# Performance work log

Measured on AMD Instinct MI355X. Metric: run time of the kernel, lower is better.

The kernel has to match this reference:

```python
import jax, jax.numpy as jnp
import numpy as np

N = 100000      # nodes (PF candidates)
E = 1600000     # edges, avg degree 16
CONT = 6        # continuous features
H = 32          # hidden_dim
PDGS = [1, 2, 11, 13, 22, 130, 211]


def _p(k, shape):
    return jax.random.normal(k, shape, jnp.float32) * 0.1


def setup_inputs() -> dict:
    key = jax.random.key(0)
    ks = jax.random.split(key, 24)
    x_cont = jax.random.normal(ks[0], (N, CONT), jnp.float32)
    pdg = jnp.array(PDGS, jnp.int32)[jax.random.randint(ks[1], (N,), 0, 7)]
    sign = jax.random.randint(ks[2], (N,), 0, 2) * 2 - 1
    charge = jax.random.randint(ks[3], (N,), -1, 2)
    pv = jax.random.randint(ks[4], (N,), 0, 8)
    x_cat = jnp.stack([pdg * sign, charge, pv], axis=1).astype(jnp.int32)
    edge_index = jax.random.randint(ks[5], (2, E), 0, N, jnp.int32)
    batch = jnp.zeros((N,), jnp.int32)
    return {
        "x_cont": x_cont, "x_cat": x_cat, "edge_index": edge_index, "batch": batch,
        "W_cont": _p(ks[6], (CONT, H // 2)), "b_cont": jnp.zeros((H // 2,), jnp.float32),
        "T_chrg": _p(ks[7], (3, H // 4)), "T_pdg": _p(ks[8], (7, H // 4)), "T_pv": _p(ks[9], (8, H // 4)),
        "W_cat": _p(ks[10], (3 * H // 4, H // 2)), "b_cat": jnp.zeros((H // 2,), jnp.float32),
        "W_enc": _p(ks[11], (H, H)), "b_enc": jnp.zeros((H,), jnp.float32),
        "g_all": jnp.ones((H,), jnp.float32), "be_all": jnp.zeros((H,), jnp.float32),
        "W_msg": _p(ks[12], (2 * H, H)), "b_msg": jnp.zeros((H,), jnp.float32),
        "g_conv": jnp.ones((H,), jnp.float32), "be_conv": jnp.zeros((H,), jnp.float32),
        "W_out1": _p(ks[13], (H, H // 2)), "b_out1": jnp.zeros((H // 2,), jnp.float32),
        "W_out2": _p(ks[14], (H // 2, 1)), "b_out2": jnp.zeros((1,), jnp.float32),
    }


def _batchnorm(x, gamma, beta, eps=1e-5):
    # training-mode BatchNorm1d: biased batch stats over the node axis
    mu = jnp.mean(x, axis=0)
    var = jnp.mean(jnp.square(x - mu), axis=0)
    return (x - mu) * jax.lax.rsqrt(var + eps) * gamma + beta


def reference(x_cont, x_cat, edge_index, batch,
              W_cont, b_cont, T_chrg, T_pdg, T_pv, W_cat, b_cat,
              W_enc, b_enc, g_all, be_all, W_msg, b_msg, g_conv, be_conv,
              W_out1, b_out1, W_out2, b_out2):
    elu = jax.nn.elu
    emb_cont = elu(x_cont @ W_cont + b_cont)                      # [N, H/2]
    emb_chrg = T_chrg[x_cat[:, 1] + 1]                            # [N, H/4]
    emb_pv = T_pv[x_cat[:, 2]]                                    # [N, H/4]
    pdg_remap = jnp.abs(x_cat[:, 0])
    for i, pdgval in enumerate(PDGS):  # fixed small constant loop, as in original
        pdg_remap = jnp.where(pdg_remap == pdgval, jnp.int32(i), pdg_remap)
    emb_pdg = T_pdg[pdg_remap]                                    # [N, H/4]
    emb_cat = elu(jnp.concatenate([emb_chrg, emb_pdg, emb_pv], axis=1) @ W_cat + b_cat)
    emb = elu(jnp.concatenate([emb_cat, emb_cont], axis=1) @ W_enc + b_enc)
    emb = _batchnorm(emb, g_all, be_all)                          # [N, H]
    # EdgeConv: m_ij = nn([x_i, x_j - x_i]), aggregate by max over incoming edges
    src, dst = edge_index[0], edge_index[1]
    x_i = emb[dst]
    x_j = emb[src]
    msg = jnp.concatenate([x_i, x_j - x_i], axis=1) @ W_msg + b_msg   # [E, H]
    agg = jax.ops.segment_max(msg, dst, num_segments=N)
    agg = jnp.where(jnp.isfinite(agg), agg, 0.0)                  # nodes w/o in-edges -> 0
    emb = emb + _batchnorm(agg, g_conv, be_conv)
    out = elu(emb @ W_out1 + b_out1) @ W_out2 + b_out2            # [N, 1]
    return out.squeeze(-1)
```

## Files before the change

### kernel.cpp

```cpp
#include <hip/hip_runtime.h>
#include <hip/hip_bf16.h>

#define NN 100000
#define EE 1600000
#define NB_SCAN 391

#define NBUCK 782
#define CPAD  16
#define NCB   128
#define NPART 391
#define NE4   400000
#define BCAP  2560

typedef __hip_bfloat16 bf16_t;
typedef int int4v __attribute__((ext_vector_type(4)));
typedef float f4 __attribute__((ext_vector_type(4)));

#define PARB  600000
#define EMB   604480
#define PBUF  3804480
#define QBUF  7004480
#define ABUF  10204480
#define SOFF  13404480
#define CURS  (SOFF + 256)
#define BASEO (CURS + 12512)
#define ROWP  (BASEO + 1024)
#define SRCL  (ROWP + 100002)

#define O_WCONT 0
#define O_BCONT 96
#define O_TCHRG 112
#define O_TPDG  136
#define O_TPV   192
#define O_WCAT  256
#define O_BCAT  640
#define O_WENC  656
#define O_BENC  1680
#define O_GALL  1712
#define O_BEALL 1744
#define O_WMSG  1776
#define O_BMSG  3824
#define O_GCONV 3856
#define O_BECONV 3888
#define O_WOUT1 3920
#define O_BOUT1 4432
#define O_WOUT2 4448
#define O_BOUT2 4464
#define NPAR    4465

__device__ __forceinline__ float bf(unsigned short u) {
    return __uint_as_float(((unsigned)u) << 16);
}
__device__ __forceinline__ f4 elu4(f4 v) {
    f4 r;
    r.x = v.x > 0.0f ? v.x : expm1f(v.x);
    r.y = v.y > 0.0f ? v.y : expm1f(v.y);
    r.z = v.z > 0.0f ? v.z : expm1f(v.z);
    r.w = v.w > 0.0f ? v.w : expm1f(v.w);
    return r;
}
__device__ __forceinline__ f4 f4max(f4 a, f4 b) {
    f4 r;
    r.x = fmaxf(a.x, b.x); r.y = fmaxf(a.y, b.y);
    r.z = fmaxf(a.z, b.z); r.w = fmaxf(a.w, b.w);
    return r;
}

struct InitArgs {
    const void* p[19];
    const unsigned short* wdet;
    int*        flagw;
    float*      par;
    int*        curs;
    float*      stats;
};

__global__ __launch_bounds__(256) void k_init(InitArgs a)
{
    const int offs[20] = {O_WCONT,O_BCONT,O_TCHRG,O_TPDG,O_TPV,O_WCAT,O_BCAT,O_WENC,
                          O_BENC,O_GALL,O_BEALL,O_WMSG,O_BMSG,O_GCONV,O_BECONV,
                          O_WOUT1,O_BOUT1,O_WOUT2,O_BOUT2,NPAR};
    __shared__ int sflag;
    int b = blockIdx.x, tid = threadIdx.x;
    int g = b * 256 + tid;
    if (g < NBUCK * CPAD) a.curs[g] = 0;
    if (g < 128) a.stats[g] = 0.0f;
    if (b == 0) {
        if (tid == 0) sflag = 0;
        __syncthreads();
        int bad = 0;
        for (int i = tid; i < 1024; i += 256) {
            unsigned e = (a.wdet[i] >> 7) & 0xFFu;
            if (e >= 137u) bad = 1;
        }
        if (bad) atomicOr(&sflag, 1);
        __syncthreads();
        int f32 = sflag;
        if (tid == 0) *a.flagw = f32;
        for (int i = tid; i < NPAR; i += 256) {
            int t = 0;
            while (offs[t + 1] <= i) t++;
            int l = i - offs[t];
            const void* s = a.p[t];
            a.par[i] = f32 ? ((const float*)s)[l] : bf(((const unsigned short*)s)[l]);
        }
    }
}

__global__ __launch_bounds__(256, 1) void k_fusedA(
    const int* __restrict__ eidx, int* __restrict__ curs,
    const void* __restrict__ xc, const int* __restrict__ x_cat,
    const float* __restrict__ par, const int* __restrict__ flag,
    float* __restrict__ emb)
{
    __shared__ f4 sWc4[24];
    __shared__ f4 sbc4[4];
    __shared__ f4 sTc4[6], sTp4[14], sTv4[16];
    __shared__ f4 sWcat4[96];
    __shared__ f4 sbcat4[4];
    __shared__ f4 sWe4[256];
    __shared__ f4 sbe4[8];
    int tid = threadIdx.x;
    int b = blockIdx.x;

    if (b < NCB) {
        __shared__ int cnt[NBUCK];
        for (int i = tid; i < NBUCK; i += 256) cnt[i] = 0;
        __syncthreads();
        const int4v* dst4 = (const int4v*)(eidx + EE);
        int i0 = b * (NE4 / NCB);
        int i1 = i0 + (NE4 / NCB);
        for (int i = i0 + tid; i < i1; i += 256) {
            int4v d = __builtin_nontemporal_load(&dst4[i]);
            atomicAdd(&cnt[d.x >> 7], 1);
            atomicAdd(&cnt[d.y >> 7], 1);
            atomicAdd(&cnt[d.z >> 7], 1);
            atomicAdd(&cnt[d.w >> 7], 1);
        }
        __syncthreads();
        for (int i = tid; i < NBUCK; i += 256) {
            int c = cnt[i];
            if (c) atomicAdd(&curs[i * CPAD], c);
        }
        return;
    }

    {
        float* s;
        s=(float*)sWc4;   for(int i=tid;i<96;  i+=256) s[i]=par[O_WCONT+i];
        s=(float*)sbc4;   for(int i=tid;i<16;  i+=256) s[i]=par[O_BCONT+i];
        s=(float*)sTc4;   for(int i=tid;i<24;  i+=256) s[i]=par[O_TCHRG+i];
        s=(float*)sTp4;   for(int i=tid;i<56;  i+=256) s[i]=par[O_TPDG+i];
        s=(float*)sTv4;   for(int i=tid;i<64;  i+=256) s[i]=par[O_TPV+i];
        s=(float*)sWcat4; for(int i=tid;i<384; i+=256) s[i]=par[O_WCAT+i];
        s=(float*)sbcat4; for(int i=tid;i<16;  i+=256) s[i]=par[O_BCAT+i];
        s=(float*)sWe4;   for(int i=tid;i<1024;i+=256) s[i]=par[O_WENC+i];
        s=(float*)sbe4;   for(int i=tid;i<32;  i+=256) s[i]=par[O_BENC+i];
    }
    __syncthreads();

    int n = (b - NCB) * 256 + tid;
    if (n >= NN) return;

    float x0,x1,x2,x3,x4,x5;
    if (*flag) {
        const float* xr = (const float*)xc + (size_t)n * 6;
        x0=xr[0]; x1=xr[1]; x2=xr[2]; x3=xr[3]; x4=xr[4]; x5=xr[5];
    } else {
        const unsigned* xr = (const unsigned*)xc + (size_t)n * 3;
        unsigned w0=xr[0], w1=xr[1], w2=xr[2];
        x0=__uint_as_float(w0<<16); x1=__uint_as_float(w0 & 0xFFFF0000u);
        x2=__uint_as_float(w1<<16); x3=__uint_as_float(w1 & 0xFFFF0000u);
        x4=__uint_as_float(w2<<16); x5=__uint_as_float(w2 & 0xFFFF0000u);
    }

    f4 ec[4];
    #pragma unroll
    for (int g = 0; g < 4; g++) {
        f4 a = sbc4[g];
        a += x0 * sWc4[0*4+g]; a += x1 * sWc4[1*4+g]; a += x2 * sWc4[2*4+g];
        a += x3 * sWc4[3*4+g]; a += x4 * sWc4[4*4+g]; a += x5 * sWc4[5*4+g];
        ec[g] = elu4(a);
    }

    int c0 = x_cat[n*3+0], c1 = x_cat[n*3+1], c2 = x_cat[n*3+2];
    int a0 = c0 < 0 ? -c0 : c0;
    int pi = (a0==1)?0:(a0==2)?1:(a0==11)?2:(a0==13)?3:(a0==22)?4:(a0==130)?5:6;
    int ci = c1 + 1;

    f4 t0a = sTc4[ci*2],  t0b = sTc4[ci*2+1];
    f4 t1a = sTp4[pi*2],  t1b = sTp4[pi*2+1];
    f4 t2a = sTv4[c2*2],  t2b = sTv4[c2*2+1];

    f4 ecat[4];
    #pragma unroll
    for (int g = 0; g < 4; g++) {
        f4 a = sbcat4[g];
        #pragma unroll
        for (int k = 0; k < 4; k++) a += t0a[k] * sWcat4[(k     )*4+g];
        #pragma unroll
        for (int k = 0; k < 4; k++) a += t0b[k] * sWcat4[(4 + k )*4+g];
        #pragma unroll
        for (int k = 0; k < 4; k++) a += t1a[k] * sWcat4[(8 + k )*4+g];
        #pragma unroll
        for (int k = 0; k < 4; k++) a += t1b[k] * sWcat4[(12 + k)*4+g];
        #pragma unroll
        for (int k = 0; k < 4; k++) a += t2a[k] * sWcat4[(16 + k)*4+g];
        #pragma unroll
        for (int k = 0; k < 4; k++) a += t2b[k] * sWcat4[(20 + k)*4+g];
        ecat[g] = elu4(a);
    }

    f4* o = (f4*)(emb + (size_t)n * 32);
    #pragma unroll
    for (int cg = 0; cg < 8; cg++) {
        f4 a = sbe4[cg];
        #pragma unroll
        for (int kg = 0; kg < 4; kg++) {
            #pragma unroll
            for (int k = 0; k < 4; k++)
                a += ecat[kg][k] * sWe4[(kg*4+k)*8 + cg];
        }
        #pragma unroll
        for (int kg = 0; kg < 4; kg++) {
            #pragma unroll
            for (int k = 0; k < 4; k++)
                a += ec[kg][k] * sWe4[(16 + kg*4+k)*8 + cg];
        }
        o[cg] = elu4(a);
    }
}

__global__ __launch_bounds__(1024) void k_scan782(int* __restrict__ curs,
                                                  int* __restrict__ base,
                                                  int* __restrict__ rowp)
{
    __shared__ int s[1024];
    int tid = threadIdx.x;
    int v = (tid < NBUCK) ? curs[tid * CPAD] : 0;
    s[tid] = v;
    __syncthreads();
    for (int off = 1; off < 1024; off <<= 1) {
        int x = (tid >= off) ? s[tid - off] : 0;
        __syncthreads();
        s[tid] += x;
        __syncthreads();
    }
    if (tid < NBUCK) {
        int bexc = s[tid] - v;
        base[tid] = bexc;
        curs[tid * CPAD] = bexc;
    }
    if (tid == NBUCK - 1) base[NBUCK] = s[tid];
    if (tid == 0) rowp[NN] = EE;
}

__global__ __launch_bounds__(256, 1) void k_partition(
    const int* __restrict__ eidx, int* __restrict__ curs, int* __restrict__ pe)
{
    __shared__ int cnt[NBUCK];
    __shared__ int start[NBUCK];
    int tid = threadIdx.x;
    int b = blockIdx.x;
    for (int i = tid; i < NBUCK; i += 256) cnt[i] = 0;
    __syncthreads();

    const int4v* src4 = (const int4v*)eidx;
    const int4v* dst4 = (const int4v*)(eidx + EE);
    int i0 = b << 10;
    int i1 = i0 + 1024; if (i1 > NE4) i1 = NE4;

    for (int i = i0 + tid; i < i1; i += 256) {
        int4v d = dst4[i];
        atomicAdd(&cnt[d.x >> 7], 1);
        atomicAdd(&cnt[d.y >> 7], 1);
        atomicAdd(&cnt[d.z >> 7], 1);
        atomicAdd(&cnt[d.w >> 7], 1);
    }
    __syncthreads();
    for (int i = tid; i < NBUCK; i += 256) {
        int c = cnt[i];
        start[i] = c ? atomicAdd(&curs[i * CPAD], c) : 0;
    }
    __syncthreads();
    for (int i = tid; i < NBUCK; i += 256) cnt[i] = 0;
    __syncthreads();
    for (int i = i0 + tid; i < i1; i += 256) {
        int4v s = src4[i];
        int4v d = dst4[i];
        int bk, r;
        bk = d.x >> 7; r = atomicAdd(&cnt[bk], 1); pe[start[bk] + r] = (s.x << 7) | (d.x & 127);
        bk = d.y >> 7; r = atomicAdd(&cnt[bk], 1); pe[start[bk] + r] = (s.y << 7) | (d.y & 127);
        bk = d.z >> 7; r = atomicAdd(&cnt[bk], 1); pe[start[bk] + r] = (s.z << 7) | (d.z & 127);
        bk = d.w >> 7; r = atomicAdd(&cnt[bk], 1); pe[start[bk] + r] = (s.w << 7) | (d.w & 127);
    }
}

__global__ __launch_bounds__(256) void k_fusedB(
    const int* __restrict__ cbase, const int* __restrict__ pe,
    int* __restrict__ rowp, int* __restrict__ srcl,
    const float* __restrict__ emb, float* __restrict__ stats)
{
    __shared__ int stage[BCAP];
    __shared__ int cnt[128], sc[128], ex[128];
    __shared__ float ls[64];
    int tid = threadIdx.x;
    int b = blockIdx.x;
    if (b < NBUCK) {
        int beg = cbase[b], end = cbase[b + 1];
        int m = end - beg;
        if (tid < 128) cnt[tid] = 0;
        __syncthreads();
        for (int i = tid; i < m; i += 256) {
            int p = pe[beg + i];
            if (i < BCAP) stage[i] = p;
            atomicAdd(&cnt[p & 127], 1);
        }
        __syncthreads();
        if (tid < 128) sc[tid] = cnt[tid];
        __syncthreads();
        for (int off = 1; off < 128; off <<= 1) {
            int x = (tid >= off && tid < 128) ? sc[tid - off] : 0;
            __syncthreads();
            if (tid < 128) sc[tid] += x;
            __syncthreads();
        }
        if (tid < 128) {
            int e0 = sc[tid] - cnt[tid];
            ex[tid] = e0;
            int node = b * 128 + tid;
            if (node < NN) rowp[node] = beg + e0;
            cnt[tid] = 0;
        }
        __syncthreads();
        for (int i = tid; i < m; i += 256) {
            int p = (i < BCAP) ? stage[i] : pe[beg + i];
            int dl = p & 127;
            int r = atomicAdd(&cnt[dl], 1);
            srcl[beg + ex[dl] + r] = p >> 7;
        }
        return;
    }
    if (tid < 64) ls[tid] = 0.0f;
    __syncthreads();
    int sb = b - NBUCK;
    int idx = sb * 256 + tid;
    int stride = 512 * 256;
    int c = idx & 31;
    float sum = 0.0f, q = 0.0f;
    for (int i = idx; i < NN * 32; i += stride) {
        float v = emb[i];
        sum += v; q += v * v;
    }
    sum += __shfl_xor(sum, 32);
    q   += __shfl_xor(q, 32);
    if ((tid & 63) < 32) {
        atomicAdd(&ls[c], sum);
        atomicAdd(&ls[32 + c], q);
    }
    __syncthreads();
    if (tid < 64) atomicAdd(&stats[tid], ls[tid]);
}

__global__ __launch_bounds__(256, 1) void k_fusedC(
    const float* __restrict__ par, const float* __restrict__ stats,
    const float* __restrict__ emb, float* __restrict__ P, float* __restrict__ Q)
{
    __shared__ f4 sWP4[256], sWQ4[256];
    __shared__ f4 sbP4[8], sbQ4[8];
    __shared__ float ssc[32], ssh[32];
    int tid = threadIdx.x;
    int b = blockIdx.x;
    if (tid < 32) {
        float mu  = stats[tid] * (1.0f / NN);
        float var = stats[32 + tid] * (1.0f / NN) - mu * mu;
        float s   = par[O_GALL + tid] * rsqrtf(var + 1e-5f);
        ssc[tid] = s;
        ssh[tid] = par[O_BEALL + tid] - mu * s;
    }
    __syncthreads();
    {
        float* wp = (float*)sWP4;
        float* wq = (float*)sWQ4;
        for (int e = tid; e < 1024; e += 256) {
            int k = e >> 5;
            float w1 = par[O_WMSG + e];
            float w2 = par[O_WMSG + 1024 + e];
            wp[e] = ssc[k] * (w1 - w2);
            wq[e] = ssc[k] * w2;
        }
    }
    if (tid < 32) {
        float aP = par[O_BMSG + tid], aQ = 0.0f;
        for (int k = 0; k < 32; k++) {
            float w1 = par[O_WMSG + k*32 + tid];
            float w2 = par[O_WMSG + (k+32)*32 + tid];
            aP += ssh[k] * (w1 - w2);
            aQ += ssh[k] * w2;
        }
        ((float*)sbP4)[tid] = aP;
        ((float*)sbQ4)[tid] = aQ;
    }
    __syncthreads();

    int n = b * 256 + tid;
    if (n >= NN) return;

    const f4* er = (const f4*)(emb + (size_t)n * 32);
    f4 e[8];
    #pragma unroll
    for (int g = 0; g < 8; g++) e[g] = er[g];

    f4* pr = (f4*)(P + (size_t)n * 32);
    f4* qr = (f4*)(Q + (size_t)n * 32);
    #pragma unroll
    for (int cg = 0; cg < 8; cg++) {
        f4 aP = sbP4[cg];
        f4 aQ = sbQ4[cg];
        #pragma unroll
        for (int kg = 0; kg < 8; kg++) {
            #pragma unroll
            for (int k = 0; k < 4; k++) {
                float ek = e[kg][k];
                aP += ek * sWP4[(kg*4+k)*8 + cg];
                aQ += ek * sWQ4[(kg*4+k)*8 + cg];
            }
        }
        pr[cg] = aP;
        qr[cg] = aQ;
    }
}

__global__ __launch_bounds__(256) void k_gather(
    const int* __restrict__ rowp, const int* __restrict__ srcl,
    const float* __restrict__ Q, const float* __restrict__ P,
    float* __restrict__ agg)
{
    int tid = threadIdx.x;
    int lane = tid & 63;
    int wave = tid >> 6;
    int n = blockIdx.x * 4 + wave;
    int slice = lane >> 3;
    int cg    = lane & 7;
    int beg = rowp[n], end = rowp[n + 1];
    const f4* Q4 = (const f4*)Q;

    f4 pv = (f4){0.f, 0.f, 0.f, 0.f};
    if (lane < 8 && end > beg) pv = ((const f4*)P)[(size_t)n * 8 + lane];

    f4 m = {-INFINITY, -INFINITY, -INFINITY, -INFINITY};
    for (int e = beg + slice; e < end; e += 32) {
        int e1 = min(e + 8,  end - 1);
        int e2 = min(e + 16, end - 1);
        int e3 = min(e + 24, end - 1);
        int s0 = __builtin_nontemporal_load(&srcl[e]);
        int s1 = __builtin_nontemporal_load(&srcl[e1]);
        int s2 = __builtin_nontemporal_load(&srcl[e2]);
        int s3 = __builtin_nontemporal_load(&srcl[e3]);
        f4 q0 = Q4[(size_t)s0 * 8 + cg];
        f4 q1 = Q4[(size_t)s1 * 8 + cg];
        f4 q2 = Q4[(size_t)s2 * 8 + cg];
        f4 q3 = Q4[(size_t)s3 * 8 + cg];
        q0 = f4max(q0, q1);
        q2 = f4max(q2, q3);
        m = f4max(m, f4max(q0, q2));
    }
    #pragma unroll
    for (int off = 8; off < 64; off <<= 1) {
        m.x = fmaxf(m.x, __shfl_xor(m.x, off));
        m.y = fmaxf(m.y, __shfl_xor(m.y, off));
        m.z = fmaxf(m.z, __shfl_xor(m.z, off));
        m.w = fmaxf(m.w, __shfl_xor(m.w, off));
    }
    if (lane < 8) {
        f4 o;
        if (end > beg) o = m + pv;
        else           o = (f4){0.f, 0.f, 0.f, 0.f};
        ((f4*)agg)[(size_t)n * 8 + lane] = o;
    }
}

__global__ __launch_bounds__(256) void k_stats(const float* __restrict__ xin,
                                               float* __restrict__ outsums, int count)
{
    __shared__ float ls[64];
    int tid = threadIdx.x;
    if (tid < 64) ls[tid] = 0.0f;
    __syncthreads();
    int idx = blockIdx.x * 256 + tid;
    int stride = gridDim.x * 256;
    int c = idx & 31;
    float s = 0.0f, q = 0.0f;
    for (int i = idx; i < count; i += stride) {
        float v = xin[i];
        s += v; q += v * v;
    }
    s += __shfl_xor(s, 32);
    q += __shfl_xor(q, 32);
    if ((tid & 63) < 32) {
        atomicAdd(&ls[c], s);
        atomicAdd(&ls[32 + c], q);
    }
    __syncthreads();
    if (tid < 64) atomicAdd(&outsums[tid], ls[tid]);
}

__global__ __launch_bounds__(256, 1) void k_out(
    const float* __restrict__ emb, const float* __restrict__ agg,
    const float* __restrict__ par, const float* __restrict__ stats,
    const int* __restrict__ flag, void* __restrict__ out)
{
    __shared__ f4 sW14[128];
    __shared__ f4 sb14[4], sW24[4];
    __shared__ f4 sc14[8], sh14[8], sc24[8], sh24[8];
    __shared__ float sb2s;
    int tid = threadIdx.x;
    {
        float* s = (float*)sW14;
        for (int i = tid; i < 512; i += 256) s[i] = par[O_WOUT1 + i];
    }
    if (tid < 16) {
        ((float*)sb14)[tid] = par[O_BOUT1 + tid];
        ((float*)sW24)[tid] = par[O_WOUT2 + tid];
    }
    if (tid < 32) {
        float mu  = stats[tid] * (1.0f / NN);
        float var = stats[32 + tid] * (1.0f / NN) - mu * mu;
        float s   = par[O_GALL + tid] * rsqrtf(var + 1e-5f);
        ((float*)sc14)[tid] = s;
        ((float*)sh14)[tid] = par[O_BEALL + tid] - mu * s;
        float mu2  = stats[64 + tid] * (1.0f / NN);
        float var2 = stats[96 + tid] * (1.0f / NN) - mu2 * mu2;
        float s2   = par[O_GCONV + tid] * rsqrtf(var2 + 1e-5f);
        ((float*)sc24)[tid] = s2;
        ((float*)sh24)[tid] = par[O_BECONV + tid] - mu2 * s2;
    }
    if (tid == 0) sb2s = par[O_BOUT2];
    __syncthreads();

    int n = blockIdx.x * 256 + tid;
    if (n >= NN) return;

    const f4* er = (const f4*)(emb + (size_t)n * 32);
    const f4* ar = (const f4*)(agg + (size_t)n * 32);
    f4 h[8];
    #pragma unroll
    for (int g = 0; g < 8; g++) {
        f4 ev = er[g];
        f4 av = ar[g];
        h[g] = ev * sc14[g] + sh14[g] + av * sc24[g] + sh24[g];
    }
    f4 o1[4];
    #pragma unroll
    for (int g = 0; g < 4; g++) {
        f4 acc = sb14[g];
        #pragma unroll
        for (int kg = 0; kg < 8; kg++) {
            #pragma unroll
            for (int k = 0; k < 4; k++)
                acc += h[kg][k] * sW14[(kg*4+k)*4 + g];
        }
        o1[g] = elu4(acc);
    }
    float acc = sb2s;
    #pragma unroll
    for (int g = 0; g < 4; g++) {
        f4 p = o1[g] * sW24[g];
        acc += p.x + p.y + p.z + p.w;
    }

    if (*flag) ((float*)out)[n] = acc;
    else       ((bf16_t*)out)[n] = __float2bfloat16(acc);
}

extern "C" void kernel_launch(void* const* d_in, const int* in_sizes, int n_in,
                              void* d_out, int out_size, void* d_ws, size_t ws_size,
                              hipStream_t stream)
{
    const void* x_cont = d_in[0];
    const int* x_cat = (const int*)d_in[1];
    const int* eidx  = (const int*)d_in[2];

    float* ws    = (float*)d_ws;
    float* par   = ws + PARB;
    float* emb   = ws + EMB;
    float* P     = ws + PBUF;
    float* Q     = ws + QBUF;
    float* agg   = ws + ABUF;
    int*   pe    = (int*)(ws + ABUF);
    float* stats = ws + SOFF;
    int*   flag  = (int*)(stats + 128);
    int*   curs  = (int*)(ws + CURS);
    int*   base  = (int*)(ws + BASEO);
    int*   rowp  = (int*)(ws + ROWP);
    int*   srcl  = (int*)(ws + SRCL);

    InitArgs ia;
    for (int t = 0; t < 19; t++) ia.p[t] = d_in[4 + t];
    ia.wdet = (const unsigned short*)d_in[11];
    ia.flagw = flag; ia.par = par; ia.curs = curs; ia.stats = stats;
    k_init<<<NB_SCAN, 256, 0, stream>>>(ia);

    k_fusedA<<<NCB + NB_SCAN, 256, 0, stream>>>(eidx, curs, x_cont, x_cat,
                                                par, flag, emb);
    k_scan782<<<1, 1024, 0, stream>>>(curs, base, rowp);
    k_partition<<<NPART, 256, 0, stream>>>(eidx, curs, pe);
    k_fusedB<<<NBUCK + 512, 256, 0, stream>>>(base, pe, rowp, srcl, emb, stats);
    k_fusedC<<<NB_SCAN, 256, 0, stream>>>(par, stats, emb, P, Q);
    k_gather<<<NN / 4, 256, 0, stream>>>(rowp, srcl, Q, P, agg);
    k_stats<<<512, 256, 0, stream>>>(agg, stats + 64, NN * 32);
    k_out<<<NB_SCAN, 256, 0, stream>>>(emb, agg, par, stats, flag, d_out);
}
```

Baseline: 294.5 us.

## Fuse edge partition with embedding and fold BN stats into producers

Replaces the separate count, scan and partition passes with a single-pass partition into fixed-capacity buckets (4096 slots each), with an atomic overflow list handled later. Embedding BatchNorm stats are computed inside the embedding kernel, and the aggregate stats are accumulated in the gather kernel into 64 partial slots. CSR build is merged with the P/Q precompute, so the pipeline goes from nine launches to five. The risks are an overflow-list scan that every bucket block must walk, extra shared and global atomics, and int2 row pointers.

```diff
diff --git a/kernel.cpp b/kernel.cpp
--- a/kernel.cpp
+++ b/kernel.cpp
@@ -7,9 +7,10 @@
 
 #define NBUCK 782
 #define CPAD  16
-#define NCB   128
 #define NPART 391
 #define NE4   400000
+#define CAP   4096
+#define CAPSH 12
 #define BCAP  2560
 
 typedef __hip_bfloat16 bf16_t;
@@ -22,10 +23,12 @@
 #define QBUF  7004480
 #define ABUF  10204480
 #define SOFF  13404480
-#define CURS  (SOFF + 256)
-#define BASEO (CURS + 12512)
-#define ROWP  (BASEO + 1024)
-#define SRCL  (ROWP + 100002)
+#define PART2 (SOFF + 256)
+#define CURS  (PART2 + 4096)
+#define ROWP2 (CURS + 12512)
+#define OFLB  (ROWP2 + 200000)
+#define PEB   (OFLB + 3200004)
+#define SRCB  (PEB + 3203072)
 
 #define O_WCONT 0
 #define O_BCONT 96
@@ -73,6 +76,9 @@
     float*      par;
     int*        curs;
     float*      stats;
+    float*      part;
+    int*        ofl;
+    int*        tcur;
 };
 
 __global__ __launch_bounds__(256) void k_init(InitArgs a)
@@ -83,8 +89,10 @@
     __shared__ int sflag;
     int b = blockIdx.x, tid = threadIdx.x;
     int g = b * 256 + tid;
-    if (g < NBUCK * CPAD) a.curs[g] = 0;
+    if (g < NBUCK) a.curs[g * CPAD] = g << CAPSH;
+    if (g < 4096) a.part[g] = 0.0f;
     if (g < 128) a.stats[g] = 0.0f;
+    if (g == 0) { a.ofl[0] = 0; *a.tcur = NBUCK << CAPSH; }
     if (b == 0) {
         if (tid == 0) sflag = 0;
         __syncthreads();
@@ -107,310 +115,295 @@
     }
 }
 
-__global__ __launch_bounds__(256, 1) void k_fusedA(
+struct SMemPart { int cnt[NBUCK]; int start[NBUCK]; };
+struct SMemEmb  { float wc[96], bc[16], tc[24], tp[56], tv[64],
+                  wcat[384], bcat[16], we[1024], be[32], ls[64]; };
+union SMemA { SMemPart p; SMemEmb e; };
+
+__global__ __launch_bounds__(256, 1) void k_fA(
     const int* __restrict__ eidx, int* __restrict__ curs,
+    int* __restrict__ pe, int* __restrict__ ofl, int2* __restrict__ ofl2,
     const void* __restrict__ xc, const int* __restrict__ x_cat,
     const float* __restrict__ par, const int* __restrict__ flag,
-    float* __restrict__ emb)
+    float* __restrict__ emb, float* __restrict__ stats)
 {
-    __shared__ f4 sWc4[24];
-    __shared__ f4 sbc4[4];
-    __shared__ f4 sTc4[6], sTp4[14], sTv4[16];
-    __shared__ f4 sWcat4[96];
-    __shared__ f4 sbcat4[4];
-    __shared__ f4 sWe4[256];
-    __shared__ f4 sbe4[8];
+    __shared__ alignas(16) SMemA sm;
     int tid = threadIdx.x;
     int b = blockIdx.x;
 
-    if (b < NCB) {
-        __shared__ int cnt[NBUCK];
-        for (int i = tid; i < NBUCK; i += 256) cnt[i] = 0;
-        __syncthreads();
+    if (b < NPART) {
+        for (int i = tid; i < NBUCK; i += 256) sm.p.cnt[i] = 0;
+        __syncthreads();
+        const int4v* src4 = (const int4v*)eidx;
         const int4v* dst4 = (const int4v*)(eidx + EE);
-        int i0 = b * (NE4 / NCB);
-        int i1 = i0 + (NE4 / NCB);
+        int i0 = b << 10;
+        int i1 = i0 + 1024; if (i1 > NE4) i1 = NE4;
         for (int i = i0 + tid; i < i1; i += 256) {
-            int4v d = __builtin_nontemporal_load(&dst4[i]);
-            atomicAdd(&cnt[d.x >> 7], 1);
-            atomicAdd(&cnt[d.y >> 7], 1);
-            atomicAdd(&cnt[d.z >> 7], 1);
-            atomicAdd(&cnt[d.w >> 7], 1);
+            int4v d = dst4[i];
+            atomicAdd(&sm.p.cnt[d.x >> 7], 1);
+            atomicAdd(&sm.p.cnt[d.y >> 7], 1);
+            atomicAdd(&sm.p.cnt[d.z >> 7], 1);
+            atomicAdd(&sm.p.cnt[d.w >> 7], 1);
         }
         __syncthreads();
         for (int i = tid; i < NBUCK; i += 256) {
-            int c = cnt[i];
-            if (c) atomicAdd(&curs[i * CPAD], c);
+            int c = sm.p.cnt[i];
+            sm.p.start[i] = c ? atomicAdd(&curs[i * CPAD], c) : 0;
+        }
+        __syncthreads();
+        for (int i = tid; i < NBUCK; i += 256) sm.p.cnt[i] = 0;
+        __syncthreads();
+        for (int i = i0 + tid; i < i1; i += 256) {
+            int4v s = src4[i];
+            int4v d = dst4[i];
+            #define PLACE(SS, DD) { \
+                int bk = (DD) >> 7; \
+                int r = atomicAdd(&sm.p.cnt[bk], 1); \
+                int slot = sm.p.start[bk] + r; \
+                int packed = ((SS) << 7) | ((DD) & 127); \
+                if (slot < ((bk + 1) << CAPSH)) pe[slot] = packed; \
+                else { int oi = atomicAdd(ofl, 1); ofl2[oi] = make_int2(bk, packed); } }
+            PLACE(s.x, d.x) PLACE(s.y, d.y) PLACE(s.z, d.z) PLACE(s.w, d.w)
+            #undef PLACE
         }
         return;
     }
 
     {
         float* s;
-        s=(float*)sWc4;   for(int i=tid;i<96;  i+=256) s[i]=par[O_WCONT+i];
-        s=(float*)sbc4;   for(int i=tid;i<16;  i+=256) s[i]=par[O_BCONT+i];
-        s=(float*)sTc4;   for(int i=tid;i<24;  i+=256) s[i]=par[O_TCHRG+i];
-        s=(float*)sTp4;   for(int i=tid;i<56;  i+=256) s[i]=par[O_TPDG+i];
-        s=(float*)sTv4;   for(int i=tid;i<64;  i+=256) s[i]=par[O_TPV+i];
-        s=(float*)sWcat4; for(int i=tid;i<384; i+=256) s[i]=par[O_WCAT+i];
-        s=(float*)sbcat4; for(int i=tid;i<16;  i+=256) s[i]=par[O_BCAT+i];
-        s=(float*)sWe4;   for(int i=tid;i<1024;i+=256) s[i]=par[O_WENC+i];
-        s=(float*)sbe4;   for(int i=tid;i<32;  i+=256) s[i]=par[O_BENC+i];
-    }
-    __syncthreads();
-
-    int n = (b - NCB) * 256 + tid;
-    if (n >= NN) return;
-
-    float x0,x1,x2,x3,x4,x5;
-    if (*flag) {
-        const float* xr = (const float*)xc + (size_t)n * 6;
-        x0=xr[0]; x1=xr[1]; x2=xr[2]; x3=xr[3]; x4=xr[4]; x5=xr[5];
-    } else {
-        const unsigned* xr = (const unsigned*)xc + (size_t)n * 3;
-        unsigned w0=xr[0], w1=xr[1], w2=xr[2];
-        x0=__uint_as_float(w0<<16); x1=__uint_as_float(w0 & 0xFFFF0000u);
-        x2=__uint_as_float(w1<<16); x3=__uint_as_float(w1 & 0xFFFF0000u);
-        x4=__uint_as_float(w2<<16); x5=__uint_as_float(w2 & 0xFFFF0000u);
-    }
-
-    f4 ec[4];
-    #pragma unroll
-    for (int g = 0; g < 4; g++) {
-        f4 a = sbc4[g];
-        a += x0 * sWc4[0*4+g]; a += x1 * sWc4[1*4+g]; a += x2 * sWc4[2*4+g];
-        a += x3 * sWc4[3*4+g]; a += x4 * sWc4[4*4+g]; a += x5 * sWc4[5*4+g];
-        ec[g] = elu4(a);
-    }
-
-    int c0 = x_cat[n*3+0], c1 = x_cat[n*3+1], c2 = x_cat[n*3+2];
-    int a0 = c0 < 0 ? -c0 : c0;
-    int pi = (a0==1)?0:(a0==2)?1:(a0==11)?2:(a0==13)?3:(a0==22)?4:(a0==130)?5:6;
-    int ci = c1 + 1;
-
-    f4 t0a = sTc4[ci*2],  t0b = sTc4[ci*2+1];
-    f4 t1a = sTp4[pi*2],  t1b = sTp4[pi*2+1];
-    f4 t2a = sTv4[c2*2],  t2b = sTv4[c2*2+1];
-
-    f4 ecat[4];
-    #pragma unroll
-    for (int g = 0; g < 4; g++) {
-        f4 a = sbcat4[g];
+        s=sm.e.wc;   for(int i=tid;i<96;  i+=256) s[i]=par[O_WCONT+i];
+        s=sm.e.bc;   for(int i=tid;i<16;  i+=256) s[i]=par[O_BCONT+i];
+        s=sm.e.tc;   for(int i=tid;i<24;  i+=256) s[i]=par[O_TCHRG+i];
+        s=sm.e.tp;   for(int i=tid;i<56;  i+=256) s[i]=par[O_TPDG+i];
+        s=sm.e.tv;   for(int i=tid;i<64;  i+=256) s[i]=par[O_TPV+i];
+        s=sm.e.wcat; for(int i=tid;i<384; i+=256) s[i]=par[O_WCAT+i];
+        s=sm.e.bcat; for(int i=tid;i<16;  i+=256) s[i]=par[O_BCAT+i];
+        s=sm.e.we;   for(int i=tid;i<1024;i+=256) s[i]=par[O_WENC+i];
+        s=sm.e.be;   for(int i=tid;i<32;  i+=256) s[i]=par[O_BENC+i];
+        if (tid < 64) sm.e.ls[tid] = 0.0f;
+    }
+    __syncthreads();
+
+    int n = (b - NPART) * 256 + tid;
+    f4 esum[8], esq[8];
+    #pragma unroll
+    for (int g = 0; g < 8; g++) { esum[g] = (f4){0,0,0,0}; esq[g] = (f4){0,0,0,0}; }
+
+    if (n < NN) {
+        f4* sWc4 = (f4*)sm.e.wc;  f4* sbc4 = (f4*)sm.e.bc;
+        f4* sTc4 = (f4*)sm.e.tc;  f4* sTp4 = (f4*)sm.e.tp;  f4* sTv4 = (f4*)sm.e.tv;
+        f4* sWcat4 = (f4*)sm.e.wcat; f4* sbcat4 = (f4*)sm.e.bcat;
+        f4* sWe4 = (f4*)sm.e.we;  f4* sbe4 = (f4*)sm.e.be;
+
+        float x0,x1,x2,x3,x4,x5;
+        if (*flag) {
+            const float* xr = (const float*)xc + (size_t)n * 6;
+            x0=xr[0]; x1=xr[1]; x2=xr[2]; x3=xr[3]; x4=xr[4]; x5=xr[5];
+        } else {
+            const unsigned* xr = (const unsigned*)xc + (size_t)n * 3;
+            unsigned w0=xr[0], w1=xr[1], w2=xr[2];
+            x0=__uint_as_float(w0<<16); x1=__uint_as_float(w0 & 0xFFFF0000u);
+            x2=__uint_as_float(w1<<16); x3=__uint_as_float(w1 & 0xFFFF0000u);
+            x4=__uint_as_float(w2<<16); x5=__uint_as_float(w2 & 0xFFFF0000u);
+        }
+
+        f4 ec[4];
         #pragma unroll
-        for (int k = 0; k < 4; k++) a += t0a[k] * sWcat4[(k     )*4+g];
+        for (int g = 0; g < 4; g++) {
+            f4 acc = sbc4[g];
+            acc += x0 * sWc4[0*4+g]; acc += x1 * sWc4[1*4+g]; acc += x2 * sWc4[2*4+g];
+            acc += x3 * sWc4[3*4+g]; acc += x4 * sWc4[4*4+g]; acc += x5 * sWc4[5*4+g];
+            ec[g] = elu4(acc);
+        }
+
+        int c0 = x_cat[n*3+0], c1 = x_cat[n*3+1], c2 = x_cat[n*3+2];
+        int a0 = c0 < 0 ? -c0 : c0;
+        int pi = (a0==1)?0:(a0==2)?1:(a0==11)?2:(a0==13)?3:(a0==22)?4:(a0==130)?5:6;
+        int ci = c1 + 1;
+
+        f4 t0a = sTc4[ci*2],  t0b = sTc4[ci*2+1];
+        f4 t1a = sTp4[pi*2],  t1b = sTp4[pi*2+1];
+        f4 t2a = sTv4[c2*2],  t2b = sTv4[c2*2+1];
+
+        f4 ecat[4];
         #pragma unroll
-        for (int k = 0; k < 4; k++) a += t0b[k] * sWcat4[(4 + k )*4+g];
+        for (int g = 0; g < 4; g++) {
+            f4 acc = sbcat4[g];
+            #pragma unroll
+            for (int k = 0; k < 4; k++) acc += t0a[k] * sWcat4[(k     )*4+g];
+            #pragma unroll
+            for (int k = 0; k < 4; k++) acc += t0b[k] * sWcat4[(4 + k )*4+g];
+            #pragma unroll
+            for (int k = 0; k < 4; k++) acc += t1a[k] * sWcat4[(8 + k )*4+g];
+            #pragma unroll
+            for (int k = 0; k < 4; k++) acc += t1b[k] * sWcat4[(12 + k)*4+g];
+            #pragma unroll
+            for (int k = 0; k < 4; k++) acc += t2a[k] * sWcat4[(16 + k)*4+g];
+            #pragma unroll
+            for (int k = 0; k < 4; k++) acc += t2b[k] * sWcat4[(20 + k)*4+g];
+            ecat[g] = elu4(acc);
+        }
+
+        f4* o = (f4*)(emb + (size_t)n * 32);
         #pragma unroll
-        for (int k = 0; k < 4; k++) a += t1a[k] * sWcat4[(8 + k )*4+g];
+        for (int cg = 0; cg < 8; cg++) {
+            f4 acc = sbe4[cg];
+            #pragma unroll
+            for (int kg = 0; kg < 4; kg++) {
+                #pragma unroll
+                for (int k = 0; k < 4; k++)
+                    acc += ecat[kg][k] * sWe4[(kg*4+k)*8 + cg];
+            }
+            #pragma unroll
+            for (int kg = 0; kg < 4; kg++) {
+                #pragma unroll
+                for (int k = 0; k < 4; k++)
+                    acc += ec[kg][k] * sWe4[(16 + kg*4+k)*8 + cg];
+            }
+            f4 v = elu4(acc);
+            o[cg] = v;
+            esum[cg] = v;
+            esq[cg]  = v * v;
+        }
+    }
+
+    #pragma unroll
+    for (int off = 1; off < 64; off <<= 1) {
         #pragma unroll
-        for (int k = 0; k < 4; k++) a += t1b[k] * sWcat4[(12 + k)*4+g];
+        for (int g = 0; g < 8; g++) {
+            esum[g].x += __shfl_xor(esum[g].x, off);
+            esum[g].y += __shfl_xor(esum[g].y, off);
+            esum[g].z += __shfl_xor(esum[g].z, off);
+            esum[g].w += __shfl_xor(esum[g].w, off);
+            esq[g].x  += __shfl_xor(esq[g].x,  off);
+            esq[g].y  += __shfl_xor(esq[g].y,  off);
+            esq[g].z  += __shfl_xor(esq[g].z,  off);
+            esq[g].w  += __shfl_xor(esq[g].w,  off);
+        }
+    }
+    if ((tid & 63) == 0) {
         #pragma unroll
-        for (int k = 0; k < 4; k++) a += t2a[k] * sWcat4[(16 + k)*4+g];
-        #pragma unroll
-        for (int k = 0; k < 4; k++) a += t2b[k] * sWcat4[(20 + k)*4+g];
-        ecat[g] = elu4(a);
-    }
-
-    f4* o = (f4*)(emb + (size_t)n * 32);
-    #pragma unroll
-    for (int cg = 0; cg < 8; cg++) {
-        f4 a = sbe4[cg];
-        #pragma unroll
-        for (int kg = 0; kg < 4; kg++) {
-            #pragma unroll
-            for (int k = 0; k < 4; k++)
-                a += ecat[kg][k] * sWe4[(kg*4+k)*8 + cg];
-        }
-        #pragma unroll
-        for (int kg = 0; kg < 4; kg++) {
-            #pragma unroll
-            for (int k = 0; k < 4; k++)
-                a += ec[kg][k] * sWe4[(16 + kg*4+k)*8 + cg];
-        }
-        o[cg] = elu4(a);
-    }
-}
-
-__global__ __launch_bounds__(1024) void k_scan782(int* __restrict__ curs,
-                                                  int* __restrict__ base,
-                                                  int* __restrict__ rowp)
+        for (int g = 0; g < 8; g++) {
+            #pragma unroll
+            for (int k = 0; k < 4; k++) {
+                atomicAdd(&sm.e.ls[g*4+k],      esum[g][k]);
+                atomicAdd(&sm.e.ls[32+g*4+k],   esq[g][k]);
+            }
+        }
+    }
+    __syncthreads();
+    if (tid < 64) atomicAdd(&stats[tid], sm.e.ls[tid]);
+}
+
+struct SMemCsr { int stage[BCAP]; int cnt[128]; int sc[128]; int ex[128]; int tl; };
+struct SMemPq  { float wp[1024], wq[1024], bp[32], bq[32], ssc[32], ssh[32]; };
+union SMemB { SMemCsr c; SMemPq q; };
+
+__global__ __launch_bounds__(256) void k_fB(
+    const int* __restrict__ curs, const int* __restrict__ pe,
+    const int* __restrict__ ofl, const int2* __restrict__ ofl2,
+    int* __restrict__ tcur, int2* __restrict__ rowp2, int* __restrict__ srcl,
+    const float* __restrict__ emb, const float* __restrict__ stats,
+    const float* __restrict__ par, float* __restrict__ P, float* __restrict__ Q)
 {
-    __shared__ int s[1024];
-    int tid = threadIdx.x;
-    int v = (tid < NBUCK) ? curs[tid * CPAD] : 0;
-    s[tid] = v;
-    __syncthreads();
-    for (int off = 1; off < 1024; off <<= 1) {
-        int x = (tid >= off) ? s[tid - off] : 0;
-        __syncthreads();
-        s[tid] += x;
-        __syncthreads();
-    }
-    if (tid < NBUCK) {
-        int bexc = s[tid] - v;
-        base[tid] = bexc;
-        curs[tid * CPAD] = bexc;
-    }
-    if (tid == NBUCK - 1) base[NBUCK] = s[tid];
-    if (tid == 0) rowp[NN] = EE;
-}
-
-__global__ __launch_bounds__(256, 1) void k_partition(
-    const int* __restrict__ eidx, int* __restrict__ curs, int* __restrict__ pe)
-{
-    __shared__ int cnt[NBUCK];
-    __shared__ int start[NBUCK];
+    __shared__ alignas(16) SMemB sm;
     int tid = threadIdx.x;
     int b = blockIdx.x;
-    for (int i = tid; i < NBUCK; i += 256) cnt[i] = 0;
-    __syncthreads();
-
-    const int4v* src4 = (const int4v*)eidx;
-    const int4v* dst4 = (const int4v*)(eidx + EE);
-    int i0 = b << 10;
-    int i1 = i0 + 1024; if (i1 > NE4) i1 = NE4;
-
-    for (int i = i0 + tid; i < i1; i += 256) {
-        int4v d = dst4[i];
-        atomicAdd(&cnt[d.x >> 7], 1);
-        atomicAdd(&cnt[d.y >> 7], 1);
-        atomicAdd(&cnt[d.z >> 7], 1);
-        atomicAdd(&cnt[d.w >> 7], 1);
-    }
-    __syncthreads();
-    for (int i = tid; i < NBUCK; i += 256) {
-        int c = cnt[i];
-        start[i] = c ? atomicAdd(&curs[i * CPAD], c) : 0;
-    }
-    __syncthreads();
-    for (int i = tid; i < NBUCK; i += 256) cnt[i] = 0;
-    __syncthreads();
-    for (int i = i0 + tid; i < i1; i += 256) {
-        int4v s = src4[i];
-        int4v d = dst4[i];
-        int bk, r;
-        bk = d.x >> 7; r = atomicAdd(&cnt[bk], 1); pe[start[bk] + r] = (s.x << 7) | (d.x & 127);
-        bk = d.y >> 7; r = atomicAdd(&cnt[bk], 1); pe[start[bk] + r] = (s.y << 7) | (d.y & 127);
-        bk = d.z >> 7; r = atomicAdd(&cnt[bk], 1); pe[start[bk] + r] = (s.z << 7) | (d.z & 127);
-        bk = d.w >> 7; r = atomicAdd(&cnt[bk], 1); pe[start[bk] + r] = (s.w << 7) | (d.w & 127);
-    }
-}
-
-__global__ __launch_bounds__(256) void k_fusedB(
-    const int* __restrict__ cbase, const int* __restrict__ pe,
-    int* __restrict__ rowp, int* __restrict__ srcl,
-    const float* __restrict__ emb, float* __restrict__ stats)
-{
-    __shared__ int stage[BCAP];
-    __shared__ int cnt[128], sc[128], ex[128];
-    __shared__ float ls[64];
-    int tid = threadIdx.x;
-    int b = blockIdx.x;
+
     if (b < NBUCK) {
-        int beg = cbase[b], end = cbase[b + 1];
-        int m = end - beg;
-        if (tid < 128) cnt[tid] = 0;
-        __syncthreads();
-        for (int i = tid; i < m; i += 256) {
+        int beg = b << CAPSH;
+        int m_res = curs[b * CPAD] - beg;
+        int stored = m_res < CAP ? m_res : CAP;
+        int no = ofl[0];
+        if (tid < 128) sm.c.cnt[tid] = 0;
+        __syncthreads();
+        for (int i = tid; i < stored; i += 256) {
             int p = pe[beg + i];
-            if (i < BCAP) stage[i] = p;
-            atomicAdd(&cnt[p & 127], 1);
-        }
-        __syncthreads();
-        if (tid < 128) sc[tid] = cnt[tid];
+            if (i < BCAP) sm.c.stage[i] = p;
+            atomicAdd(&sm.c.cnt[p & 127], 1);
+        }
+        for (int j = tid; j < no; j += 256) {
+            int2 oe = ofl2[j];
+            if (oe.x == b) atomicAdd(&sm.c.cnt[oe.y & 127], 1);
+        }
+        __syncthreads();
+        if (tid < 128) sm.c.sc[tid] = sm.c.cnt[tid];
         __syncthreads();
         for (int off = 1; off < 128; off <<= 1) {
-            int x = (tid >= off && tid < 128) ? sc[tid - off] : 0;
+            int x = (tid >= off && tid < 128) ? sm.c.sc[tid - off] : 0;
             __syncthreads();
-            if (tid < 128) sc[tid] += x;
+            if (tid < 128) sm.c.sc[tid] += x;
             __syncthreads();
         }
+        int obeg = beg;
+        if (m_res > CAP) {
+            if (tid == 0) sm.c.tl = atomicAdd(tcur, m_res);
+            __syncthreads();
+            obeg = sm.c.tl;
+        }
         if (tid < 128) {
-            int e0 = sc[tid] - cnt[tid];
-            ex[tid] = e0;
+            int e0 = sm.c.sc[tid] - sm.c.cnt[tid];
+            int deg = sm.c.cnt[tid];
+            sm.c.ex[tid] = e0;
             int node = b * 128 + tid;
-            if (node < NN) rowp[node] = beg + e0;
-            cnt[tid] = 0;
-        }
-        __syncthreads();
-        for (int i = tid; i < m; i += 256) {
-            int p = (i < BCAP) ? stage[i] : pe[beg + i];
+            if (node < NN) rowp2[node] = make_int2(obeg + e0, obeg + e0 + deg);
+            sm.c.cnt[tid] = 0;
+        }
+        __syncthreads();
+        for (int i = tid; i < stored; i += 256) {
+            int p = (i < BCAP) ? sm.c.stage[i] : pe[beg + i];
             int dl = p & 127;
-            int r = atomicAdd(&cnt[dl], 1);
-            srcl[beg + ex[dl] + r] = p >> 7;
+            int r = atomicAdd(&sm.c.cnt[dl], 1);
+            srcl[obeg + sm.c.ex[dl] + r] = p >> 7;
+        }
+        for (int j = tid; j < no; j += 256) {
+            int2 oe = ofl2[j];
+            if (oe.x == b) {
+                int dl = oe.y & 127;
+                int r = atomicAdd(&sm.c.cnt[dl], 1);
+                srcl[obeg + sm.c.ex[dl] + r] = oe.y >> 7;
+            }
         }
         return;
     }
-    if (tid < 64) ls[tid] = 0.0f;
-    __syncthreads();
-    int sb = b - NBUCK;
-    int idx = sb * 256 + tid;
-    int stride = 512 * 256;
-    int c = idx & 31;
-    float sum = 0.0f, q = 0.0f;
-    for (int i = idx; i < NN * 32; i += stride) {
-        float v = emb[i];
-        sum += v; q += v * v;
-    }
-    sum += __shfl_xor(sum, 32);
-    q   += __shfl_xor(q, 32);
-    if ((tid & 63) < 32) {
-        atomicAdd(&ls[c], sum);
-        atomicAdd(&ls[32 + c], q);
-    }
-    __syncthreads();
-    if (tid < 64) atomicAdd(&stats[tid], ls[tid]);
-}
-
-__global__ __launch_bounds__(256, 1) void k_fusedC(
-    const float* __restrict__ par, const float* __restrict__ stats,
-    const float* __restrict__ emb, float* __restrict__ P, float* __restrict__ Q)
-{
-    __shared__ f4 sWP4[256], sWQ4[256];
-    __shared__ f4 sbP4[8], sbQ4[8];
-    __shared__ float ssc[32], ssh[32];
-    int tid = threadIdx.x;
-    int b = blockIdx.x;
+
     if (tid < 32) {
         float mu  = stats[tid] * (1.0f / NN);
         float var = stats[32 + tid] * (1.0f / NN) - mu * mu;
         float s   = par[O_GALL + tid] * rsqrtf(var + 1e-5f);
-        ssc[tid] = s;
-        ssh[tid] = par[O_BEALL + tid] - mu * s;
-    }
-    __syncthreads();
-    {
-        float* wp = (float*)sWP4;
-        float* wq = (float*)sWQ4;
-        for (int e = tid; e < 1024; e += 256) {
-            int k = e >> 5;
-            float w1 = par[O_WMSG + e];
-            float w2 = par[O_WMSG + 1024 + e];
-            wp[e] = ssc[k] * (w1 - w2);
-            wq[e] = ssc[k] * w2;
-        }
+        sm.q.ssc[tid] = s;
+        sm.q.ssh[tid] = par[O_BEALL + tid] - mu * s;
+    }
+    __syncthreads();
+    for (int e = tid; e < 1024; e += 256) {
+        int k = e >> 5;
+        float w1 = par[O_WMSG + e];
+        float w2 = par[O_WMSG + 1024 + e];
+        sm.q.wp[e] = sm.q.ssc[k] * (w1 - w2);
+        sm.q.wq[e] = sm.q.ssc[k] * w2;
     }
     if (tid < 32) {
         float aP = par[O_BMSG + tid], aQ = 0.0f;
         for (int k = 0; k < 32; k++) {
             float w1 = par[O_WMSG + k*32 + tid];
             float w2 = par[O_WMSG + (k+32)*32 + tid];
-            aP += ssh[k] * (w1 - w2);
-            aQ += ssh[k] * w2;
-        }
-        ((float*)sbP4)[tid] = aP;
-        ((float*)sbQ4)[tid] = aQ;
-    }
-    __syncthreads();
-
-    int n = b * 256 + tid;
+            aP += sm.q.ssh[k] * (w1 - w2);
+            aQ += sm.q.ssh[k] * w2;
+        }
+        sm.q.bp[tid] = aP;
+        sm.q.bq[tid] = aQ;
+    }
+    __syncthreads();
+
+    int n = (b - NBUCK) * 256 + tid;
     if (n >= NN) return;
 
+    f4* sWP4 = (f4*)sm.q.wp; f4* sWQ4 = (f4*)sm.q.wq;
+    f4* sbP4 = (f4*)sm.q.bp; f4* sbQ4 = (f4*)sm.q.bq;
     const f4* er = (const f4*)(emb + (size_t)n * 32);
     f4 e[8];
     #pragma unroll
     for (int g = 0; g < 8; g++) e[g] = er[g];
-
     f4* pr = (f4*)(P + (size_t)n * 32);
     f4* qr = (f4*)(Q + (size_t)n * 32);
     #pragma unroll
@@ -432,17 +425,22 @@
 }
 
 __global__ __launch_bounds__(256) void k_gather(
-    const int* __restrict__ rowp, const int* __restrict__ srcl,
+    const int2* __restrict__ rowp2, const int* __restrict__ srcl,
     const float* __restrict__ Q, const float* __restrict__ P,
-    float* __restrict__ agg)
+    float* __restrict__ agg, float* __restrict__ part)
 {
+    __shared__ float ls[64];
     int tid = threadIdx.x;
+    if (tid < 64) ls[tid] = 0.0f;
+    __syncthreads();
+
     int lane = tid & 63;
     int wave = tid >> 6;
     int n = blockIdx.x * 4 + wave;
     int slice = lane >> 3;
     int cg    = lane & 7;
-    int beg = rowp[n], end = rowp[n + 1];
+    int2 be = rowp2[n];
+    int beg = be.x, end = be.y;
     const f4* Q4 = (const f4*)Q;
 
     f4 pv = (f4){0.f, 0.f, 0.f, 0.f};
@@ -477,42 +475,29 @@
         if (end > beg) o = m + pv;
         else           o = (f4){0.f, 0.f, 0.f, 0.f};
         ((f4*)agg)[(size_t)n * 8 + lane] = o;
-    }
-}
-
-__global__ __launch_bounds__(256) void k_stats(const float* __restrict__ xin,
-                                               float* __restrict__ outsums, int count)
-{
-    __shared__ float ls[64];
-    int tid = threadIdx.x;
-    if (tid < 64) ls[tid] = 0.0f;
-    __syncthreads();
-    int idx = blockIdx.x * 256 + tid;
-    int stride = gridDim.x * 256;
-    int c = idx & 31;
-    float s = 0.0f, q = 0.0f;
-    for (int i = idx; i < count; i += stride) {
-        float v = xin[i];
-        s += v; q += v * v;
-    }
-    s += __shfl_xor(s, 32);
-    q += __shfl_xor(q, 32);
-    if ((tid & 63) < 32) {
-        atomicAdd(&ls[c], s);
-        atomicAdd(&ls[32 + c], q);
-    }
-    __syncthreads();
-    if (tid < 64) atomicAdd(&outsums[tid], ls[tid]);
+        atomicAdd(&ls[cg*4+0], o.x);
+        atomicAdd(&ls[cg*4+1], o.y);
+        atomicAdd(&ls[cg*4+2], o.z);
+        atomicAdd(&ls[cg*4+3], o.w);
+        atomicAdd(&ls[32+cg*4+0], o.x*o.x);
+        atomicAdd(&ls[32+cg*4+1], o.y*o.y);
+        atomicAdd(&ls[32+cg*4+2], o.z*o.z);
+        atomicAdd(&ls[32+cg*4+3], o.w*o.w);
+    }
+    __syncthreads();
+    if (tid < 64) atomicAdd(&part[(blockIdx.x & 63) * 64 + tid], ls[tid]);
 }
 
 __global__ __launch_bounds__(256, 1) void k_out(
     const float* __restrict__ emb, const float* __restrict__ agg,
     const float* __restrict__ par, const float* __restrict__ stats,
+    const float* __restrict__ part,
     const int* __restrict__ flag, void* __restrict__ out)
 {
     __shared__ f4 sW14[128];
     __shared__ f4 sb14[4], sW24[4];
     __shared__ f4 sc14[8], sh14[8], sc24[8], sh24[8];
+    __shared__ float spart[64];
     __shared__ float sb2s;
     int tid = threadIdx.x;
     {
@@ -523,19 +508,26 @@
         ((float*)sb14)[tid] = par[O_BOUT1 + tid];
         ((float*)sW24)[tid] = par[O_WOUT2 + tid];
     }
+    if (tid < 64) {
+        float acc2 = 0.0f;
+        #pragma unroll 8
+        for (int r = 0; r < 64; r++) acc2 += part[r * 64 + tid];
+        spart[tid] = acc2;
+    }
+    if (tid == 0) sb2s = par[O_BOUT2];
+    __syncthreads();
     if (tid < 32) {
         float mu  = stats[tid] * (1.0f / NN);
         float var = stats[32 + tid] * (1.0f / NN) - mu * mu;
         float s   = par[O_GALL + tid] * rsqrtf(var + 1e-5f);
         ((float*)sc14)[tid] = s;
         ((float*)sh14)[tid] = par[O_BEALL + tid] - mu * s;
-        float mu2  = stats[64 + tid] * (1.0f / NN);
-        float var2 = stats[96 + tid] * (1.0f / NN) - mu2 * mu2;
+        float mu2  = spart[tid] * (1.0f / NN);
+        float var2 = spart[32 + tid] * (1.0f / NN) - mu2 * mu2;
         float s2   = par[O_GCONV + tid] * rsqrtf(var2 + 1e-5f);
         ((float*)sc24)[tid] = s2;
         ((float*)sh24)[tid] = par[O_BECONV + tid] - mu2 * s2;
     }
-    if (tid == 0) sb2s = par[O_BOUT2];
     __syncthreads();
 
     int n = blockIdx.x * 256 + tid;
@@ -572,6 +564,7 @@
     if (*flag) ((float*)out)[n] = acc;
     else       ((bf16_t*)out)[n] = __float2bfloat16(acc);
 }
+
 
 extern "C" void kernel_launch(void* const* d_in, const int* in_sizes, int n_in,
                               void* d_out, int out_size, void* d_ws, size_t ws_size,
@@ -587,27 +580,28 @@
     float* P     = ws + PBUF;
     float* Q     = ws + QBUF;
     float* agg   = ws + ABUF;
-    int*   pe    = (int*)(ws + ABUF);
     float* stats = ws + SOFF;
     int*   flag  = (int*)(stats + 128);
+    float* part  = ws + PART2;
     int*   curs  = (int*)(ws + CURS);
-    int*   base  = (int*)(ws + BASEO);
-    int*   rowp  = (int*)(ws + ROWP);
-    int*   srcl  = (int*)(ws + SRCL);
+    int2*  rowp2 = (int2*)(ws + ROWP2);
+    int*   ofl   = (int*)(ws + OFLB);
+    int2*  ofl2  = (int2*)(ws + OFLB + 2);
+    int*   pe    = (int*)(ws + PEB);
+    int*   srcl  = (int*)(ws + SRCB);
+    int*   tcur  = (int*)(stats + 130);
 
     InitArgs ia;
     for (int t = 0; t < 19; t++) ia.p[t] = d_in[4 + t];
     ia.wdet = (const unsigned short*)d_in[11];
     ia.flagw = flag; ia.par = par; ia.curs = curs; ia.stats = stats;
+    ia.part = part; ia.ofl = ofl; ia.tcur = tcur;
     k_init<<<NB_SCAN, 256, 0, stream>>>(ia);
 
-    k_fusedA<<<NCB + NB_SCAN, 256, 0, stream>>>(eidx, curs, x_cont, x_cat,
-                                                par, flag, emb);
-    k_scan782<<<1, 1024, 0, stream>>>(curs, base, rowp);
-    k_partition<<<NPART, 256, 0, stream>>>(eidx, curs, pe);
-    k_fusedB<<<NBUCK + 512, 256, 0, stream>>>(base, pe, rowp, srcl, emb, stats);
-    k_fusedC<<<NB_SCAN, 256, 0, stream>>>(par, stats, emb, P, Q);
-    k_gather<<<NN / 4, 256, 0, stream>>>(rowp, srcl, Q, P, agg);
-    k_stats<<<512, 256, 0, stream>>>(agg, stats + 64, NN * 32);
-    k_out<<<NB_SCAN, 256, 0, stream>>>(emb, agg, par, stats, flag, d_out);
-}
+    k_fA<<<NPART + NB_SCAN, 256, 0, stream>>>(eidx, curs, pe, ofl, ofl2,
+                                              x_cont, x_cat, par, flag, emb, stats);
+    k_fB<<<NBUCK + NB_SCAN, 256, 0, stream>>>(curs, pe, ofl, ofl2, tcur, rowp2, srcl,
+                                              emb, stats, par, P, Q);
+    k_gather<<<NN / 4, 256, 0, stream>>>(rowp2, srcl, Q, P, agg, part);
+    k_out<<<NB_SCAN, 256, 0, stream>>>(emb, agg, par, stats, part, flag, d_out);
+}
```

Result: faster. 286.0 us (-2.9%).
